# Kernel tuning notes

Hardware: AMD Instinct MI355X
Metric: run time of the kernel (lower is better)

The kernel has to match this reference:

```python
import jax, jax.numpy as jnp
import numpy as np

D_MODEL = 1024
D_STATE = 32
EXPAND = 2
D_INNER = D_MODEL * EXPAND
B_SZ = 2
SEQ = 512


def setup_inputs() -> dict:
    key = jax.random.key(0)
    ks = jax.random.split(key, 10)
    x = jax.random.normal(ks[0], (B_SZ, SEQ, D_MODEL), dtype=jnp.float32)
    W_in = jax.random.normal(ks[1], (2 * D_INNER, D_MODEL), dtype=jnp.float32) * 0.02
    A_log = jax.random.uniform(ks[2], (D_INNER, D_STATE), minval=-4.0, maxval=-1.0, dtype=jnp.float32)
    W_B = jax.random.normal(ks[3], (D_STATE, D_MODEL), dtype=jnp.float32) * 0.02
    W_C = jax.random.normal(ks[4], (D_STATE, D_MODEL), dtype=jnp.float32) * 0.02
    W_dt = jax.random.normal(ks[5], (D_INNER, D_MODEL), dtype=jnp.float32) * 0.02
    b_dt = jnp.zeros((D_INNER,), dtype=jnp.float32)
    dt_bias = jnp.zeros((D_INNER,), dtype=jnp.float32) - 4.0
    rope_freq = jax.random.normal(ks[6], (D_STATE // 2,), dtype=jnp.float32) * 0.01
    ln_w = jnp.ones((D_INNER,), dtype=jnp.float32)
    ln_b = jnp.zeros((D_INNER,), dtype=jnp.float32)
    W_out = jax.random.normal(ks[7], (D_MODEL, D_INNER), dtype=jnp.float32) * 0.02
    return {"x": x, "W_in": W_in, "A_log": A_log, "W_B": W_B, "W_C": W_C,
            "W_dt": W_dt, "b_dt": b_dt, "dt_bias": dt_bias, "rope_freq": rope_freq,
            "ln_w": ln_w, "ln_b": ln_b, "W_out": W_out}


def _forward(x, W_in, A_log, W_B, W_C, W_dt, b_dt, dt_bias, rope_freq, ln_w, ln_b, W_out):
    B, L, _ = x.shape
    half = D_STATE // 2
    offset = 0

    xz = jnp.einsum('bld,ed->ble', x, W_in)                 # [B,L,2*D_INNER]
    x_inner = xz[..., :D_INNER]                             # [B,L,DI]
    z = jax.nn.silu(xz[..., D_INNER:])                      # [B,L,DI]

    A = -jnp.exp(A_log)                                     # [DI,DS]
    Bm = jnp.einsum('bld,nd->bln', x, W_B)                  # [B,L,DS]
    Cm = jnp.einsum('bld,nd->bln', x, W_C)                  # [B,L,DS]
    dt = jax.nn.softplus(jnp.einsum('bld,ed->ble', x, W_dt) + b_dt + dt_bias)  # [B,L,DI]

    # trapezoidal discretization
    dtA = dt[..., None] * A                                 # [B,L,DI,DS]
    denom = 1.0 - dtA / 2.0
    A_bar = (1.0 + dtA / 2.0) / denom                       # [B,L,DI,DS]
    B_bar = dt[..., None] / denom                           # [B,L,DI,DS]

    # per-step rope rotation angles: angle_t = rope_freq * (t + offset)
    t_idx = jnp.arange(L, dtype=jnp.float32) + offset       # [L]
    ang = t_idx[:, None] * rope_freq                        # [L,half]
    cos_a = jnp.cos(ang)
    sin_a = jnp.sin(ang)

    def step(state, inp):
        A_t, Bb_t, B_t, x_t, C_t, c_t, s_t = inp
        # state update: [B,DI,DS]
        state = A_t * state + Bb_t * B_t[:, None, :] * x_t[:, :, None]
        real = state[..., :half]
        imag = state[..., half:]
        state = jnp.concatenate([real * c_t - imag * s_t,
                                 real * s_t + imag * c_t], axis=-1)
        y_t = jnp.einsum('bds,bs->bd', state, C_t)          # [B,DI]
        return state, y_t

    state0 = jnp.zeros((B, D_INNER, D_STATE), dtype=x.dtype)
    xs = (jnp.swapaxes(A_bar, 0, 1), jnp.swapaxes(B_bar, 0, 1),
          jnp.swapaxes(Bm, 0, 1), jnp.swapaxes(x_inner, 0, 1),
          jnp.swapaxes(Cm, 0, 1), cos_a, sin_a)
    final_state, ys = jax.lax.scan(step, state0, xs)        # ys: [L,B,DI]
    out = jnp.swapaxes(ys, 0, 1) * z                        # [B,L,DI]

    # LayerNorm over last dim (eps=1e-5, torch default)
    mu = jnp.mean(out, axis=-1, keepdims=True)
    var = jnp.mean((out - mu) ** 2, axis=-1, keepdims=True)
    out = (out - mu) * jax.lax.rsqrt(var + 1e-5) * ln_w + ln_b

    out = jnp.einsum('ble,de->bld', out, W_out)             # [B,L,D_MODEL]
    return out, final_state


def reference(x, W_in, A_log, W_B, W_C, W_dt, b_dt, dt_bias, rope_freq, ln_w, ln_b, W_out):
    return _forward(x, W_in, A_log, W_B, W_C, W_dt, b_dt, dt_bias, rope_freq, ln_w, ln_b, W_out)
```

## Files before the change

### kernel.cpp

```cpp
#include <hip/hip_runtime.h>
#include <math.h>

#define B_SZ 2
#define SEQ 512
#define DM 1024
#define DI 2048
#define DS 32
#define TOK (B_SZ*SEQ)
#define NCH 8
#define CLEN (SEQ/NCH)
#define NPAIRH 32768

#define NFUSED 6272

typedef float v2f __attribute__((ext_vector_type(2)));

__device__ __forceinline__ unsigned short f2bf(float f) {
  unsigned int u = __builtin_bit_cast(unsigned int, f);
  unsigned int r = u + 0x7fffu + ((u >> 16) & 1u);
  return (unsigned short)(r >> 16);
}

template<int CTRL>
__device__ __forceinline__ float row_ror_add(float x) {
  int s = __builtin_amdgcn_update_dpp(0, __builtin_bit_cast(int, x), CTRL, 0xf, 0xf, false);
  return x + __builtin_bit_cast(float, s);
}
__device__ __forceinline__ float row16_sum(float v) {
  v = row_ror_add<0x121>(v);
  v = row_ror_add<0x122>(v);
  v = row_ror_add<0x124>(v);
  v = row_ror_add<0x128>(v);
  return v;
}

__global__ __launch_bounds__(256) void fused_cast(const float* __restrict__ x,
                                                  const float* __restrict__ W_in,
                                                  const float* __restrict__ W_dt,
                                                  const float* __restrict__ W_B,
                                                  const float* __restrict__ W_C,
                                                  const float* __restrict__ W_out,
                                                  unsigned short* __restrict__ xb,
                                                  unsigned short* __restrict__ wcat,
                                                  unsigned short* __restrict__ wob) {
  int g = blockIdx.x * 256 + threadIdx.x;
  const float* s; unsigned short* dd; int off;
  if      (g <  131072) { s = x;     dd = xb;             off = 0; }
  else if (g <  655360) { s = W_in;  dd = wcat;           off = 131072; }
  else if (g <  917504) { s = W_dt;  dd = wcat + 4194304; off = 655360; }
  else if (g <  921600) { s = W_B;   dd = wcat + 6291456; off = 917504; }
  else if (g <  925696) { s = W_C;   dd = wcat + 6324224; off = 921600; }
  else if (g < 1187840) { s = W_out; dd = wob;            off = 925696; }
  else return;
  int i = g - off;
  float4 a = ((const float4*)s)[i * 2];
  float4 b = ((const float4*)s)[i * 2 + 1];
  union { unsigned short us[8]; uint4 v; } o;
  o.us[0] = f2bf(a.x); o.us[1] = f2bf(a.y); o.us[2] = f2bf(a.z); o.us[3] = f2bf(a.w);
  o.us[4] = f2bf(b.x); o.us[5] = f2bf(b.y); o.us[6] = f2bf(b.z); o.us[7] = f2bf(b.w);
  ((uint4*)dd)[i] = o.v;
}

typedef __attribute__((ext_vector_type(8))) short  frag8;
typedef __attribute__((ext_vector_type(4))) float  facc4;

__device__ __forceinline__ void gload_lds16(const unsigned short* g, unsigned short* l) {
  __builtin_amdgcn_global_load_lds((const __attribute__((address_space(1))) unsigned int*)g,
                                   (__attribute__((address_space(3))) unsigned int*)l, 16, 0, 0);
}
__device__ __forceinline__ void gload_lds16f(const float* g, float* l) {
  __builtin_amdgcn_global_load_lds((const __attribute__((address_space(1))) unsigned int*)g,
                                   (__attribute__((address_space(3))) unsigned int*)l, 16, 0, 0);
}

__device__ __forceinline__ float softplus_fast(float v) {
  return fmaxf(v, 0.f) + __logf(1.f + __expf(-fabsf(v)));
}

__global__ __launch_bounds__(256) void gemm1_big(const unsigned short* __restrict__ A,
                                                 const unsigned short* __restrict__ Bw,
                                                 float* __restrict__ o_xs,
                                                 float* __restrict__ o_zb,
                                                 float* __restrict__ o_dts,
                                                 float* __restrict__ o_bcb,
                                                 const float* __restrict__ b_dt,
                                                 const float* __restrict__ dt_bias) {
  __shared__ __align__(16) unsigned short As[128 * 64];
  __shared__ __align__(16) unsigned short Bs[64 * 64];
  const int K = DM;
  const int tid = threadIdx.x;
  const int w = tid >> 6, lane = tid & 63;
  const int wm = w >> 1, wn = w & 1;
  const int bid = blockIdx.x;
  const int Wk = (bid & 7) * 98 + (bid >> 3);
  const int m0 = (Wk & 7) * 128;
  const int n0 = (Wk >> 3) * 64;
  const int r = lane & 15, q = lane >> 4;
  const int srow = lane >> 3;
  const int scol = ((lane & 7) ^ srow) * 8;
  facc4 acc[4][2] = {};
  const unsigned short* Ag = A + (size_t)m0 * K;
  const unsigned short* Bg = Bw + (size_t)n0 * K;

  for (int k0 = 0; k0 < DM; k0 += 64) {
#pragma unroll
    for (int k = 0; k < 4; ++k) {
      int ch = w * 4 + k;
      gload_lds16(Ag + (size_t)(ch * 8 + srow) * K + k0 + scol, &As[ch * 512]);
    }
#pragma unroll
    for (int k = 0; k < 2; ++k) {
      int ch = w * 2 + k;
      gload_lds16(Bg + (size_t)(ch * 8 + srow) * K + k0 + scol, &Bs[ch * 512]);
    }
    __syncthreads();
#pragma unroll
    for (int kk = 0; kk < 2; ++kk) {
      frag8 af[4], bfr[2];
      const int sw = ((kk * 4 + q) ^ (r & 7)) * 8;
#pragma unroll
      for (int i = 0; i < 4; ++i)
        af[i] = *(const frag8*)&As[(wm * 64 + i * 16 + r) * 64 + sw];
#pragma unroll
      for (int jj = 0; jj < 2; ++jj)
        bfr[jj] = *(const frag8*)&Bs[(wn * 32 + jj * 16 + r) * 64 + sw];
#pragma unroll
      for (int i = 0; i < 4; ++i)
#pragma unroll
        for (int jj = 0; jj < 2; ++jj)
          acc[i][jj] = __builtin_amdgcn_mfma_f32_16x16x32_bf16(af[i], bfr[jj], acc[i][jj], 0, 0, 0);
    }
    __syncthreads();
  }

#pragma unroll
  for (int i = 0; i < 4; ++i) {
#pragma unroll
    for (int jj = 0; jj < 2; ++jj) {
      int n = n0 + wn * 32 + jj * 16 + r;
      int mb = m0 + wm * 64 + i * 16 + q * 4;
      if (n < 2048) {
#pragma unroll
        for (int rg = 0; rg < 4; ++rg)
          o_xs[(size_t)(mb + rg) * DI + n] = acc[i][jj][rg];
      } else if (n < 4096) {
#pragma unroll
        for (int rg = 0; rg < 4; ++rg)
          o_zb[(size_t)(mb + rg) * DI + (n - 2048)] = acc[i][jj][rg];
      } else if (n < 6144) {
        int d = n - 4096;
        float bias = b_dt[d] + dt_bias[d];
#pragma unroll
        for (int rg = 0; rg < 4; ++rg)
          o_dts[(size_t)(mb + rg) * DI + d] = softplus_fast(acc[i][jj][rg] + bias);
      } else if (n < 6176) {
#pragma unroll
        for (int rg = 0; rg < 4; ++rg)
          o_bcb[(size_t)(mb + rg) * DS + (n - 6144)] = acc[i][jj][rg];
      } else if (n < 6208) {
#pragma unroll
        for (int rg = 0; rg < 4; ++rg)
          o_bcb[(size_t)TOK * DS + (size_t)(mb + rg) * DS + (n - 6176)] = acc[i][jj][rg];
      }
    }
  }
}

template<int MT, int NT, int KSP, bool ROUTE>
__global__ __launch_bounds__(256) void gemm_mfma(const unsigned short* __restrict__ A,
                                                 const unsigned short* __restrict__ Bw,
                                                 int K,
                                                 float* __restrict__ o_xs,
                                                 float* __restrict__ o_zb,
                                                 float* __restrict__ o_dts,
                                                 float* __restrict__ o_bcb,
                                                 const float* __restrict__ b_dt,
                                                 const float* __restrict__ dt_bias,
                                                 float* __restrict__ o_c, int ldc) {
  __shared__ __align__(16) unsigned short As[64 * 64];
  __shared__ __align__(16) unsigned short Bs[64 * 64];
  const int tid = threadIdx.x;
  const int w = tid >> 6, lane = tid & 63;
  const int wm = w >> 1, wn = w & 1;
  const int bid = blockIdx.x;
  const int Wk = (bid & 7) * ((int)gridDim.x >> 3) + (bid >> 3);
  const int ks = Wk / (MT * NT);
  const int rem = Wk % (MT * NT);
  const int m0 = (rem % MT) * 64;
  const int n0 = (rem / MT) * 64;
  const int kLen = K / KSP, kBeg = ks * kLen;
  const int r = lane & 15, q = lane >> 4;
  const int srow = lane >> 3;
  const int scol = ((lane & 7) ^ (srow & 7)) * 8;
  facc4 acc[2][2] = {};
  const unsigned short* Ag = A + (size_t)m0 * K + kBeg;
  const unsigned short* Bg = Bw + (size_t)n0 * K + kBeg;

  for (int k0 = 0; k0 < kLen; k0 += 64) {
#pragma unroll
    for (int k = 0; k < 2; ++k) {
      int ch = w * 2 + k;
      gload_lds16(Ag + (size_t)(ch * 8 + srow) * K + k0 + scol, &As[ch * 512]);
      gload_lds16(Bg + (size_t)(ch * 8 + srow) * K + k0 + scol, &Bs[ch * 512]);
    }
    __syncthreads();
#pragma unroll
    for (int kk = 0; kk < 2; ++kk) {
      frag8 af[2], bf[2];
      const int sw = ((kk * 4 + q) ^ (r & 7)) * 8;
#pragma unroll
      for (int i = 0; i < 2; ++i)
        af[i] = *(const frag8*)&As[(wm * 32 + i * 16 + r) * 64 + sw];
#pragma unroll
      for (int jj = 0; jj < 2; ++jj)
        bf[jj] = *(const frag8*)&Bs[(wn * 32 + jj * 16 + r) * 64 + sw];
#pragma unroll
      for (int i = 0; i < 2; ++i)
#pragma unroll
        for (int jj = 0; jj < 2; ++jj)
          acc[i][jj] = __builtin_amdgcn_mfma_f32_16x16x32_bf16(af[i], bf[jj], acc[i][jj], 0, 0, 0);
    }
    __syncthreads();
  }

#pragma unroll
  for (int i = 0; i < 2; ++i) {
#pragma unroll
    for (int jj = 0; jj < 2; ++jj) {
      int n = n0 + wn * 32 + jj * 16 + r;
      int mb = m0 + wm * 32 + i * 16 + q * 4;
      if (ROUTE) {
        if (n < 2048) {
#pragma unroll
          for (int rg = 0; rg < 4; ++rg)
            o_xs[(size_t)(mb + rg) * DI + n] = acc[i][jj][rg];
        } else if (n < 4096) {
#pragma unroll
          for (int rg = 0; rg < 4; ++rg)
            o_zb[(size_t)(mb + rg) * DI + (n - 2048)] = acc[i][jj][rg];
        } else if (n < 6144) {
          int d = n - 4096;
          float bias = b_dt[d] + dt_bias[d];
#pragma unroll
          for (int rg = 0; rg < 4; ++rg)
            o_dts[(size_t)(mb + rg) * DI + d] = softplus_fast(acc[i][jj][rg] + bias);
        } else if (n < 6176) {
#pragma unroll
          for (int rg = 0; rg < 4; ++rg)
            o_bcb[(size_t)(mb + rg) * DS + (n - 6144)] = acc[i][jj][rg];
        } else if (n < 6208) {
#pragma unroll
          for (int rg = 0; rg < 4; ++rg)
            o_bcb[(size_t)TOK * DS + (size_t)(mb + rg) * DS + (n - 6176)] = acc[i][jj][rg];
        }
      } else {
        float* oc = o_c + (size_t)ks * (MT * 64) * ldc;
#pragma unroll
        for (int rg = 0; rg < 4; ++rg)
          oc[(size_t)(mb + rg) * ldc + n] = acc[i][jj][rg];
      }
    }
  }
}

__global__ __launch_bounds__(256) void addk(const float* __restrict__ p0,
                                            const float* __restrict__ p1,
                                            float* __restrict__ o) {
  int i = blockIdx.x * 256 + threadIdx.x;
  float4 a = ((const float4*)p0)[i];
  float4 b = ((const float4*)p1)[i];
  ((float4*)o)[i] = make_float4(a.x + b.x, a.y + b.y, a.z + b.z, a.w + b.w);
}

__global__ __launch_bounds__(256) void scan_p1(const float* __restrict__ xs,
                                               const float* __restrict__ dts,
                                               const float* __restrict__ bcb,
                                               const float* __restrict__ A_log,
                                               const float* __restrict__ rope,
                                               float* __restrict__ Pbuf) {
  __shared__ __align__(16) float lds[6144];
  const int blk = blockIdx.x;
  const int c = blk >> 7;
  const int sub = blk & 127;
  const int b = sub >> 6;
  const int dbase = (sub & 63) << 5;
  const int tid = threadIdx.x;
  const int wv = tid >> 6, lane = tid & 63;
  const int j = tid & 15;
  const int ca = (tid >> 4) & 15;
  const int l0 = c * CLEN;
  const size_t base = (size_t)(b * SEQ + l0);

  {
    int row = wv * 16 + (lane >> 3);
    int col = (lane & 7) << 2;
#pragma unroll
    for (int k = 0; k < 2; ++k) {
      gload_lds16f(xs  + (base + row + k * 8) * DI + dbase + col, &lds[(wv * 16 + k * 8) * 32]);
      gload_lds16f(dts + (base + row + k * 8) * DI + dbase + col, &lds[2048 + (wv * 16 + k * 8) * 32]);
    }
#pragma unroll
    for (int k = 0; k < 2; ++k) {
      int seg = wv * 2 + k;
      gload_lds16f(bcb + base * DS + seg * 256 + lane * 4, &lds[4096 + seg * 256]);
    }
  }

  const int dA = dbase + 2 * ca;
  v2f Ar, Ai;
  Ar.x = -0.5f * expf(A_log[dA * DS + j]);
  Ar.y = -0.5f * expf(A_log[(dA + 1) * DS + j]);
  Ai.x = -0.5f * expf(A_log[dA * DS + j + 16]);
  Ai.y = -0.5f * expf(A_log[(dA + 1) * DS + j + 16]);
  const float fr = rope[j];
  float sn, cs, sF, cF;
  sincosf((float)l0 * fr, &sn, &cs);
  sincosf(fr, &sF, &cF);
  __syncthreads();

  v2f p00 = {1.f, 1.f}, p01 = {0.f, 0.f}, p10 = {0.f, 0.f}, p11 = {1.f, 1.f};
  v2f ur = {0.f, 0.f}, ui = {0.f, 0.f};

#pragma unroll 4
  for (int tt = 0; tt < CLEN; ++tt) {
    const int ro = tt * 32;
    v2f xin = *(const v2f*)&lds[ro + 2 * ca];
    v2f dtd = *(const v2f*)&lds[2048 + ro + 2 * ca];
    float Br = lds[4096 + ro + j];
    float Bi = lds[4096 + ro + j + 16];
    v2f hr = dtd * Ar, hi = dtd * Ai;
    v2f invr, invi;
    invr.x = __builtin_amdgcn_rcpf(1.f - hr.x);
    invr.y = __builtin_amdgcn_rcpf(1.f - hr.y);
    invi.x = __builtin_amdgcn_rcpf(1.f - hi.x);
    invi.y = __builtin_amdgcn_rcpf(1.f - hi.y);
    v2f Abr = 2.f * invr - 1.f;
    v2f Abi = 2.f * invi - 1.f;
    v2f dx = dtd * xin;
    v2f bxr = dx * invr * Br;
    v2f bxi = dx * invi * Bi;
    v2f tr = Abr * ur + bxr;
    v2f ti = Abi * ui + bxi;
    ur = tr * cs - ti * sn;
    ui = tr * sn + ti * cs;
    v2f q00 = Abr * p00, q01 = Abr * p01;
    v2f q10 = Abi * p10, q11 = Abi * p11;
    p00 = q00 * cs - q10 * sn; p10 = q00 * sn + q10 * cs;
    p01 = q01 * cs - q11 * sn; p11 = q01 * sn + q11 * cs;
    float nc = fmaf(cs, cF, -sn * sF);
    float ns = fmaf(sn, cF,  cs * sF);
    cs = nc; sn = ns;
  }
  const int pc = (b * 1024 + (dbase >> 1) + ca) * 16 + j;
  float2* Pb2 = (float2*)Pbuf;
  Pb2[(c * 6 + 0) * NPAIRH + pc] = make_float2(p00.x, p00.y);
  Pb2[(c * 6 + 1) * NPAIRH + pc] = make_float2(p01.x, p01.y);
  Pb2[(c * 6 + 2) * NPAIRH + pc] = make_float2(p10.x, p10.y);
  Pb2[(c * 6 + 3) * NPAIRH + pc] = make_float2(p11.x, p11.y);
  Pb2[(c * 6 + 4) * NPAIRH + pc] = make_float2(ur.x, ur.y);
  Pb2[(c * 6 + 5) * NPAIRH + pc] = make_float2(ui.x, ui.y);
}

__global__ __launch_bounds__(256) void scan_p3(const float* __restrict__ xs,
                                               const float* __restrict__ dts,
                                               const float* __restrict__ bcb,
                                               const float* __restrict__ A_log,
                                               const float* __restrict__ rope,
                                               const float* __restrict__ Pbuf,
                                               float* __restrict__ y,
                                               float* __restrict__ fstate) {
  __shared__ __align__(16) float lds[8192];
  const int blk = blockIdx.x;
  const int c = blk >> 7;
  const int sub = blk & 127;
  const int b = sub >> 6;
  const int dbase = (sub & 63) << 5;
  const int tid = threadIdx.x;
  const int wv = tid >> 6, lane = tid & 63;
  const int j = tid & 15;
  const int ca = (tid >> 4) & 15;
  const int l0 = c * CLEN;
  const size_t base = (size_t)(b * SEQ + l0);

  {
    int row = wv * 16 + (lane >> 3);
    int col = (lane & 7) << 2;
#pragma unroll
    for (int k = 0; k < 2; ++k) {
      gload_lds16f(xs  + (base + row + k * 8) * DI + dbase + col, &lds[(wv * 16 + k * 8) * 32]);
      gload_lds16f(dts + (base + row + k * 8) * DI + dbase + col, &lds[2048 + (wv * 16 + k * 8) * 32]);
    }
#pragma unroll
    for (int k = 0; k < 2; ++k) {
      int seg = wv * 2 + k;
      gload_lds16f(bcb + base * DS + seg * 256 + lane * 4, &lds[4096 + seg * 256]);
      gload_lds16f(bcb + (size_t)TOK * DS + base * DS + seg * 256 + lane * 4, &lds[6144 + seg * 256]);
    }
  }

  const int dA = dbase + 2 * ca;
  v2f Ar, Ai;
  Ar.x = -0.5f * expf(A_log[dA * DS + j]);
  Ar.y = -0.5f * expf(A_log[(dA + 1) * DS + j]);
  Ai.x = -0.5f * expf(A_log[dA * DS + j + 16]);
  Ai.y = -0.5f * expf(A_log[(dA + 1) * DS + j + 16]);
  const float fr = rope[j];
  float sn, cs, sF, cF;
  sincosf((float)l0 * fr, &sn, &cs);
  sincosf(fr, &sF, &cF);

  const int pc = (b * 1024 + (dbase >> 1) + ca) * 16 + j;
  const float2* Pb2 = (const float2*)Pbuf;
  v2f sr = {0.f, 0.f}, si = {0.f, 0.f};
  for (int k = 0; k < c; ++k) {
    float2 f;
    f = Pb2[(k * 6 + 0) * NPAIRH + pc]; v2f p00 = {f.x, f.y};
    f = Pb2[(k * 6 + 1) * NPAIRH + pc]; v2f p01 = {f.x, f.y};
    f = Pb2[(k * 6 + 2) * NPAIRH + pc]; v2f p10 = {f.x, f.y};
    f = Pb2[(k * 6 + 3) * NPAIRH + pc]; v2f p11 = {f.x, f.y};
    f = Pb2[(k * 6 + 4) * NPAIRH + pc]; v2f ur  = {f.x, f.y};
    f = Pb2[(k * 6 + 5) * NPAIRH + pc]; v2f ui  = {f.x, f.y};
    v2f nr = p00 * sr + p01 * si + ur;
    v2f ni = p10 * sr + p11 * si + ui;
    sr = nr; si = ni;
  }
  __syncthreads();

  float* yp = y + base * DI + dA;

#pragma unroll 4
  for (int tt = 0; tt < CLEN; ++tt) {
    const int ro = tt * 32;
    v2f xin = *(const v2f*)&lds[ro + 2 * ca];
    v2f dtd = *(const v2f*)&lds[2048 + ro + 2 * ca];
    float Br = lds[4096 + ro + j];
    float Bi = lds[4096 + ro + j + 16];
    float Cr = lds[6144 + ro + j];
    float Ci = lds[6144 + ro + j + 16];
    v2f hr = dtd * Ar, hi = dtd * Ai;
    v2f invr, invi;
    invr.x = __builtin_amdgcn_rcpf(1.f - hr.x);
    invr.y = __builtin_amdgcn_rcpf(1.f - hr.y);
    invi.x = __builtin_amdgcn_rcpf(1.f - hi.x);
    invi.y = __builtin_amdgcn_rcpf(1.f - hi.y);
    v2f Abr = 2.f * invr - 1.f;
    v2f Abi = 2.f * invi - 1.f;
    v2f dx = dtd * xin;
    v2f bxr = dx * invr * Br;
    v2f bxi = dx * invi * Bi;
    v2f tr = Abr * sr + bxr;
    v2f ti = Abi * si + bxi;
    sr = tr * cs - ti * sn;
    si = tr * sn + ti * cs;
    v2f p = sr * Cr + si * Ci;
    float pA = row16_sum(p.x);
    float pB = row16_sum(p.y);
    if (j == 0) *(float2*)&yp[tt * DI] = make_float2(pA, pB);
    float nc = fmaf(cs, cF, -sn * sF);
    float ns = fmaf(sn, cF,  cs * sF);
    cs = nc; sn = ns;
  }
  if (c == NCH - 1) {
    fstate[((size_t)b * DI + dA) * DS + j]          = sr.x;
    fstate[((size_t)b * DI + dA) * DS + j + 16]     = si.x;
    fstate[((size_t)b * DI + dA + 1) * DS + j]      = sr.y;
    fstate[((size_t)b * DI + dA + 1) * DS + j + 16] = si.y;
  }
}

__global__ __launch_bounds__(256) void gate_ln(const float* __restrict__ y,
                                               const float* __restrict__ zb,
                                               const float* __restrict__ lw,
                                               const float* __restrict__ lb,
                                               unsigned short* __restrict__ o) {
  int tok = blockIdx.x;
  int t = threadIdx.x;
  float g[8];
  float sum = 0.f, sq = 0.f;
#pragma unroll
  for (int i = 0; i < 8; ++i) {
    int dd = t + i * 256;
    float yv = y[(size_t)tok * DI + dd];
    float zv = zb[(size_t)tok * DI + dd];
    float sg = zv / (1.f + __expf(-zv));
    float v = yv * sg;
    g[i] = v; sum += v; sq += v * v;
  }
#pragma unroll
  for (int off = 32; off; off >>= 1) { sum += __shfl_xor(sum, off); sq += __shfl_xor(sq, off); }
  __shared__ float rs[4], rq[4];
  int w = t >> 6;
  if ((t & 63) == 0) { rs[w] = sum; rq[w] = sq; }
  __syncthreads();
  sum = rs[0] + rs[1] + rs[2] + rs[3];
  sq  = rq[0] + rq[1] + rq[2] + rq[3];
  float mu = sum * (1.f / DI);
  float var = sq * (1.f / DI) - mu * mu;
  float rstd = rsqrtf(var + 1e-5f);
#pragma unroll
  for (int i = 0; i < 8; ++i) {
    int dd = t + i * 256;
    o[(size_t)tok * DI + dd] = f2bf((g[i] - mu) * rstd * lw[dd] + lb[dd]);
  }
}

extern "C" void kernel_launch(void* const* d_in, const int* in_sizes, int n_in,
                              void* d_out, int out_size, void* d_ws, size_t ws_size,
                              hipStream_t stream) {
  const float* x       = (const float*)d_in[0];
  const float* W_in    = (const float*)d_in[1];
  const float* A_log   = (const float*)d_in[2];
  const float* W_B     = (const float*)d_in[3];
  const float* W_C     = (const float*)d_in[4];
  const float* W_dt    = (const float*)d_in[5];
  const float* b_dt    = (const float*)d_in[6];
  const float* dt_bias = (const float*)d_in[7];
  const float* rope    = (const float*)d_in[8];
  const float* ln_w    = (const float*)d_in[9];
  const float* ln_b    = (const float*)d_in[10];
  const float* W_out   = (const float*)d_in[11];
  float* out = (float*)d_out;
  float* ws = (float*)d_ws;

  float* xs   = ws;
  float* zb   = ws + 2097152;
  float* dts  = ws + 4194304;
  float* bcb  = ws + 6291456;
  unsigned short* wob  = (unsigned short*)(ws + 6356992);
  unsigned short* xb   = (unsigned short*)(ws + 7405568);
  unsigned short* wcat = (unsigned short*)(ws + 7929856);
  float* Pbuf = ws + 7929856;
  float* yb   = ws + 11141120;
  unsigned short* lnb = (unsigned short*)(ws + 13238272);
  float* Pk   = ws;
  float* fstate = out + (size_t)TOK * DM;

  fused_cast<<<4640, 256, 0, stream>>>(x, W_in, W_dt, W_B, W_C, W_out, xb, wcat, wob);
  gemm1_big<<<784, 256, 0, stream>>>(xb, wcat, xs, zb, dts, bcb, b_dt, dt_bias);
  scan_p1<<<(NCH - 1) * 128, 256, 0, stream>>>(xs, dts, bcb, A_log, rope, Pbuf);
  scan_p3<<<NCH * 128, 256, 0, stream>>>(xs, dts, bcb, A_log, rope, Pbuf, yb, fstate);
  gate_ln<<<TOK, 256, 0, stream>>>(yb, zb, ln_w, ln_b, lnb);
  gemm_mfma<16, 16, 2, false><<<16 * 16 * 2, 256, 0, stream>>>(
      lnb, wob, DI, nullptr, nullptr, nullptr, nullptr, nullptr, nullptr, Pk, DM);
  addk<<<(TOK * DM) / 1024, 256, 0, stream>>>(Pk, Pk + (size_t)TOK * DM, out);
}
```

Before: 204.0 us.

## Fuse chunked scan phases into one kernel with inter-block flag synchronization

Merges the two scan kernels into a single launch. Each chunk block computes its chunk transfer matrices, publishes them to a global buffer, and raises a release flag. Later-chunk blocks spin on acquire flags to combine the prefix states before running the output pass. This removes a kernel launch and reuses the loaded tiles across both phases, but it relies on earlier blocks being scheduled before later ones to avoid deadlock. It also switches the exp and sincos setup to the fast intrinsics and drops the unused routed path from the generic GEMM.

```diff
diff --git a/kernel.cpp b/kernel.cpp
--- a/kernel.cpp
+++ b/kernel.cpp
@@ -42,7 +42,10 @@
                                                   const float* __restrict__ W_out,
                                                   unsigned short* __restrict__ xb,
                                                   unsigned short* __restrict__ wcat,
-                                                  unsigned short* __restrict__ wob) {
+                                                  unsigned short* __restrict__ wob,
+                                                  int* __restrict__ flags) {
+  if (blockIdx.x == 0 && threadIdx.x < 224)
+    ((int4*)flags)[threadIdx.x] = make_int4(0, 0, 0, 0);
   int g = blockIdx.x * 256 + threadIdx.x;
   const float* s; unsigned short* dd; int off;
   if      (g <  131072) { s = x;     dd = xb;             off = 0; }
@@ -166,16 +169,10 @@
   }
 }
 
-template<int MT, int NT, int KSP, bool ROUTE>
+template<int MT, int NT, int KSP>
 __global__ __launch_bounds__(256) void gemm_mfma(const unsigned short* __restrict__ A,
                                                  const unsigned short* __restrict__ Bw,
                                                  int K,
-                                                 float* __restrict__ o_xs,
-                                                 float* __restrict__ o_zb,
-                                                 float* __restrict__ o_dts,
-                                                 float* __restrict__ o_bcb,
-                                                 const float* __restrict__ b_dt,
-                                                 const float* __restrict__ dt_bias,
                                                  float* __restrict__ o_c, int ldc) {
   __shared__ __align__(16) unsigned short As[64 * 64];
   __shared__ __align__(16) unsigned short Bs[64 * 64];
@@ -229,36 +226,10 @@
     for (int jj = 0; jj < 2; ++jj) {
       int n = n0 + wn * 32 + jj * 16 + r;
       int mb = m0 + wm * 32 + i * 16 + q * 4;
-      if (ROUTE) {
-        if (n < 2048) {
-#pragma unroll
-          for (int rg = 0; rg < 4; ++rg)
-            o_xs[(size_t)(mb + rg) * DI + n] = acc[i][jj][rg];
-        } else if (n < 4096) {
-#pragma unroll
-          for (int rg = 0; rg < 4; ++rg)
-            o_zb[(size_t)(mb + rg) * DI + (n - 2048)] = acc[i][jj][rg];
-        } else if (n < 6144) {
-          int d = n - 4096;
-          float bias = b_dt[d] + dt_bias[d];
-#pragma unroll
-          for (int rg = 0; rg < 4; ++rg)
-            o_dts[(size_t)(mb + rg) * DI + d] = softplus_fast(acc[i][jj][rg] + bias);
-        } else if (n < 6176) {
-#pragma unroll
-          for (int rg = 0; rg < 4; ++rg)
-            o_bcb[(size_t)(mb + rg) * DS + (n - 6144)] = acc[i][jj][rg];
-        } else if (n < 6208) {
-#pragma unroll
-          for (int rg = 0; rg < 4; ++rg)
-            o_bcb[(size_t)TOK * DS + (size_t)(mb + rg) * DS + (n - 6176)] = acc[i][jj][rg];
-        }
-      } else {
-        float* oc = o_c + (size_t)ks * (MT * 64) * ldc;
-#pragma unroll
-        for (int rg = 0; rg < 4; ++rg)
-          oc[(size_t)(mb + rg) * ldc + n] = acc[i][jj][rg];
-      }
+      float* oc = o_c + (size_t)ks * (MT * 64) * ldc;
+#pragma unroll
+      for (int rg = 0; rg < 4; ++rg)
+        oc[(size_t)(mb + rg) * ldc + n] = acc[i][jj][rg];
     }
   }
 }
@@ -272,103 +243,15 @@
   ((float4*)o)[i] = make_float4(a.x + b.x, a.y + b.y, a.z + b.z, a.w + b.w);
 }
 
-__global__ __launch_bounds__(256) void scan_p1(const float* __restrict__ xs,
-                                               const float* __restrict__ dts,
-                                               const float* __restrict__ bcb,
-                                               const float* __restrict__ A_log,
-                                               const float* __restrict__ rope,
-                                               float* __restrict__ Pbuf) {
-  __shared__ __align__(16) float lds[6144];
-  const int blk = blockIdx.x;
-  const int c = blk >> 7;
-  const int sub = blk & 127;
-  const int b = sub >> 6;
-  const int dbase = (sub & 63) << 5;
-  const int tid = threadIdx.x;
-  const int wv = tid >> 6, lane = tid & 63;
-  const int j = tid & 15;
-  const int ca = (tid >> 4) & 15;
-  const int l0 = c * CLEN;
-  const size_t base = (size_t)(b * SEQ + l0);
-
-  {
-    int row = wv * 16 + (lane >> 3);
-    int col = (lane & 7) << 2;
-#pragma unroll
-    for (int k = 0; k < 2; ++k) {
-      gload_lds16f(xs  + (base + row + k * 8) * DI + dbase + col, &lds[(wv * 16 + k * 8) * 32]);
-      gload_lds16f(dts + (base + row + k * 8) * DI + dbase + col, &lds[2048 + (wv * 16 + k * 8) * 32]);
-    }
-#pragma unroll
-    for (int k = 0; k < 2; ++k) {
-      int seg = wv * 2 + k;
-      gload_lds16f(bcb + base * DS + seg * 256 + lane * 4, &lds[4096 + seg * 256]);
-    }
-  }
-
-  const int dA = dbase + 2 * ca;
-  v2f Ar, Ai;
-  Ar.x = -0.5f * expf(A_log[dA * DS + j]);
-  Ar.y = -0.5f * expf(A_log[(dA + 1) * DS + j]);
-  Ai.x = -0.5f * expf(A_log[dA * DS + j + 16]);
-  Ai.y = -0.5f * expf(A_log[(dA + 1) * DS + j + 16]);
-  const float fr = rope[j];
-  float sn, cs, sF, cF;
-  sincosf((float)l0 * fr, &sn, &cs);
-  sincosf(fr, &sF, &cF);
-  __syncthreads();
-
-  v2f p00 = {1.f, 1.f}, p01 = {0.f, 0.f}, p10 = {0.f, 0.f}, p11 = {1.f, 1.f};
-  v2f ur = {0.f, 0.f}, ui = {0.f, 0.f};
-
-#pragma unroll 4
-  for (int tt = 0; tt < CLEN; ++tt) {
-    const int ro = tt * 32;
-    v2f xin = *(const v2f*)&lds[ro + 2 * ca];
-    v2f dtd = *(const v2f*)&lds[2048 + ro + 2 * ca];
-    float Br = lds[4096 + ro + j];
-    float Bi = lds[4096 + ro + j + 16];
-    v2f hr = dtd * Ar, hi = dtd * Ai;
-    v2f invr, invi;
-    invr.x = __builtin_amdgcn_rcpf(1.f - hr.x);
-    invr.y = __builtin_amdgcn_rcpf(1.f - hr.y);
-    invi.x = __builtin_amdgcn_rcpf(1.f - hi.x);
-    invi.y = __builtin_amdgcn_rcpf(1.f - hi.y);
-    v2f Abr = 2.f * invr - 1.f;
-    v2f Abi = 2.f * invi - 1.f;
-    v2f dx = dtd * xin;
-    v2f bxr = dx * invr * Br;
-    v2f bxi = dx * invi * Bi;
-    v2f tr = Abr * ur + bxr;
-    v2f ti = Abi * ui + bxi;
-    ur = tr * cs - ti * sn;
-    ui = tr * sn + ti * cs;
-    v2f q00 = Abr * p00, q01 = Abr * p01;
-    v2f q10 = Abi * p10, q11 = Abi * p11;
-    p00 = q00 * cs - q10 * sn; p10 = q00 * sn + q10 * cs;
-    p01 = q01 * cs - q11 * sn; p11 = q01 * sn + q11 * cs;
-    float nc = fmaf(cs, cF, -sn * sF);
-    float ns = fmaf(sn, cF,  cs * sF);
-    cs = nc; sn = ns;
-  }
-  const int pc = (b * 1024 + (dbase >> 1) + ca) * 16 + j;
-  float2* Pb2 = (float2*)Pbuf;
-  Pb2[(c * 6 + 0) * NPAIRH + pc] = make_float2(p00.x, p00.y);
-  Pb2[(c * 6 + 1) * NPAIRH + pc] = make_float2(p01.x, p01.y);
-  Pb2[(c * 6 + 2) * NPAIRH + pc] = make_float2(p10.x, p10.y);
-  Pb2[(c * 6 + 3) * NPAIRH + pc] = make_float2(p11.x, p11.y);
-  Pb2[(c * 6 + 4) * NPAIRH + pc] = make_float2(ur.x, ur.y);
-  Pb2[(c * 6 + 5) * NPAIRH + pc] = make_float2(ui.x, ui.y);
-}
-
-__global__ __launch_bounds__(256) void scan_p3(const float* __restrict__ xs,
-                                               const float* __restrict__ dts,
-                                               const float* __restrict__ bcb,
-                                               const float* __restrict__ A_log,
-                                               const float* __restrict__ rope,
-                                               const float* __restrict__ Pbuf,
-                                               float* __restrict__ y,
-                                               float* __restrict__ fstate) {
+__global__ __launch_bounds__(256, 4) void scan_fused(const float* __restrict__ xs,
+                                                     const float* __restrict__ dts,
+                                                     const float* __restrict__ bcb,
+                                                     const float* __restrict__ A_log,
+                                                     const float* __restrict__ rope,
+                                                     float* __restrict__ Pbuf,
+                                                     int* __restrict__ flags,
+                                                     float* __restrict__ y,
+                                                     float* __restrict__ fstate) {
   __shared__ __align__(16) float lds[8192];
   const int blk = blockIdx.x;
   const int c = blk >> 7;
@@ -400,19 +283,69 @@
 
   const int dA = dbase + 2 * ca;
   v2f Ar, Ai;
-  Ar.x = -0.5f * expf(A_log[dA * DS + j]);
-  Ar.y = -0.5f * expf(A_log[(dA + 1) * DS + j]);
-  Ai.x = -0.5f * expf(A_log[dA * DS + j + 16]);
-  Ai.y = -0.5f * expf(A_log[(dA + 1) * DS + j + 16]);
+  Ar.x = -0.5f * __expf(A_log[dA * DS + j]);
+  Ar.y = -0.5f * __expf(A_log[(dA + 1) * DS + j]);
+  Ai.x = -0.5f * __expf(A_log[dA * DS + j + 16]);
+  Ai.y = -0.5f * __expf(A_log[(dA + 1) * DS + j + 16]);
   const float fr = rope[j];
-  float sn, cs, sF, cF;
-  sincosf((float)l0 * fr, &sn, &cs);
-  sincosf(fr, &sF, &cF);
-
+  float sn0, cs0, sF, cF;
+  __sincosf((float)l0 * fr, &sn0, &cs0);
+  __sincosf(fr, &sF, &cF);
   const int pc = (b * 1024 + (dbase >> 1) + ca) * 16 + j;
-  const float2* Pb2 = (const float2*)Pbuf;
+  float2* Pb2 = (float2*)Pbuf;
+  __syncthreads();
+
+  if (c < NCH - 1) {
+    float cs = cs0, sn = sn0;
+    v2f p00 = {1.f, 1.f}, p01 = {0.f, 0.f}, p10 = {0.f, 0.f}, p11 = {1.f, 1.f};
+    v2f ur = {0.f, 0.f}, ui = {0.f, 0.f};
+#pragma unroll 4
+    for (int tt = 0; tt < CLEN; ++tt) {
+      const int ro = tt * 32;
+      v2f xin = *(const v2f*)&lds[ro + 2 * ca];
+      v2f dtd = *(const v2f*)&lds[2048 + ro + 2 * ca];
+      float Br = lds[4096 + ro + j];
+      float Bi = lds[4096 + ro + j + 16];
+      v2f hr = dtd * Ar, hi = dtd * Ai;
+      v2f invr, invi;
+      invr.x = __builtin_amdgcn_rcpf(1.f - hr.x);
+      invr.y = __builtin_amdgcn_rcpf(1.f - hr.y);
+      invi.x = __builtin_amdgcn_rcpf(1.f - hi.x);
+      invi.y = __builtin_amdgcn_rcpf(1.f - hi.y);
+      v2f Abr = 2.f * invr - 1.f;
+      v2f Abi = 2.f * invi - 1.f;
+      v2f dx = dtd * xin;
+      v2f bxr = dx * invr * Br;
+      v2f bxi = dx * invi * Bi;
+      v2f tr = Abr * ur + bxr;
+      v2f ti = Abi * ui + bxi;
+      ur = tr * cs - ti * sn;
+      ui = tr * sn + ti * cs;
+      v2f q00 = Abr * p00, q01 = Abr * p01;
+      v2f q10 = Abi * p10, q11 = Abi * p11;
+      p00 = q00 * cs - q10 * sn; p10 = q00 * sn + q10 * cs;
+      p01 = q01 * cs - q11 * sn; p11 = q01 * sn + q11 * cs;
+      float nc = fmaf(cs, cF, -sn * sF);
+      float ns = fmaf(sn, cF,  cs * sF);
+      cs = nc; sn = ns;
+    }
+    Pb2[(c * 6 + 0) * NPAIRH + pc] = make_float2(p00.x, p00.y);
+    Pb2[(c * 6 + 1) * NPAIRH + pc] = make_float2(p01.x, p01.y);
+    Pb2[(c * 6 + 2) * NPAIRH + pc] = make_float2(p10.x, p10.y);
+    Pb2[(c * 6 + 3) * NPAIRH + pc] = make_float2(p11.x, p11.y);
+    Pb2[(c * 6 + 4) * NPAIRH + pc] = make_float2(ur.x, ur.y);
+    Pb2[(c * 6 + 5) * NPAIRH + pc] = make_float2(ui.x, ui.y);
+    __threadfence();
+    __syncthreads();
+    if (tid == 0)
+      __hip_atomic_store(&flags[blk], 1, __ATOMIC_RELEASE, __HIP_MEMORY_SCOPE_AGENT);
+  }
+
   v2f sr = {0.f, 0.f}, si = {0.f, 0.f};
   for (int k = 0; k < c; ++k) {
+    while (__hip_atomic_load(&flags[k * 128 + sub], __ATOMIC_ACQUIRE,
+                             __HIP_MEMORY_SCOPE_AGENT) == 0)
+      __builtin_amdgcn_s_sleep(2);
     float2 f;
     f = Pb2[(k * 6 + 0) * NPAIRH + pc]; v2f p00 = {f.x, f.y};
     f = Pb2[(k * 6 + 1) * NPAIRH + pc]; v2f p01 = {f.x, f.y};
@@ -424,10 +357,9 @@
     v2f ni = p10 * sr + p11 * si + ui;
     sr = nr; si = ni;
   }
-  __syncthreads();
 
   float* yp = y + base * DI + dA;
-
+  float cs = cs0, sn = sn0;
 #pragma unroll 4
   for (int tt = 0; tt < CLEN; ++tt) {
     const int ro = tt * 32;
@@ -532,15 +464,14 @@
   float* Pbuf = ws + 7929856;
   float* yb   = ws + 11141120;
   unsigned short* lnb = (unsigned short*)(ws + 13238272);
+  int*   flags = (int*)(ws + 14286848);
   float* Pk   = ws;
   float* fstate = out + (size_t)TOK * DM;
 
-  fused_cast<<<4640, 256, 0, stream>>>(x, W_in, W_dt, W_B, W_C, W_out, xb, wcat, wob);
+  fused_cast<<<4640, 256, 0, stream>>>(x, W_in, W_dt, W_B, W_C, W_out, xb, wcat, wob, flags);
   gemm1_big<<<784, 256, 0, stream>>>(xb, wcat, xs, zb, dts, bcb, b_dt, dt_bias);
-  scan_p1<<<(NCH - 1) * 128, 256, 0, stream>>>(xs, dts, bcb, A_log, rope, Pbuf);
-  scan_p3<<<NCH * 128, 256, 0, stream>>>(xs, dts, bcb, A_log, rope, Pbuf, yb, fstate);
+  scan_fused<<<NCH * 128, 256, 0, stream>>>(xs, dts, bcb, A_log, rope, Pbuf, flags, yb, fstate);
   gate_ln<<<TOK, 256, 0, stream>>>(yb, zb, ln_w, ln_b, lnb);
-  gemm_mfma<16, 16, 2, false><<<16 * 16 * 2, 256, 0, stream>>>(
-      lnb, wob, DI, nullptr, nullptr, nullptr, nullptr, nullptr, nullptr, Pk, DM);
+  gemm_mfma<16, 16, 2><<<16 * 16 * 2, 256, 0, stream>>>(lnb, wob, DI, Pk, DM);
   addk<<<(TOK * DM) / 1024, 256, 0, stream>>>(Pk, Pk + (size_t)TOK * DM, out);
 }
```

After: 394.7 us. 1.93x slower.
